# Kernel tuning notes

Hardware: AMD Instinct MI355X
Metric: run time of the kernel (lower is better)

Reference implementation:

```python
import jax, jax.numpy as jnp
import numpy as np

B, T, D = 2, 2048, 512
HEADS, DIM_HEAD, MAX_LAG = 8, 64, 5
INNER = HEADS * DIM_HEAD


def setup_inputs() -> dict:
    key = jax.random.key(0)
    k0, k1, k2, k3, k4 = jax.random.split(key, 5)
    x = jax.random.normal(k0, (B, T, D), dtype=jnp.float32)
    # Linear weights stored as (in, out); torch applies x @ W.T with W (out, in).
    Wq = jax.random.normal(k1, (D, INNER), dtype=jnp.float32) * (1.0 / np.sqrt(D))
    Wk = jax.random.normal(k2, (D, INNER), dtype=jnp.float32) * (1.0 / np.sqrt(D))
    Wv = jax.random.normal(k3, (D, INNER), dtype=jnp.float32) * (1.0 / np.sqrt(D))
    Wo = jax.random.normal(k4, (INNER, D), dtype=jnp.float32) * (1.0 / np.sqrt(INNER))
    bo = jnp.zeros((D,), dtype=jnp.float32)
    # Module's init: lag_weights = log(exp(-lags/(max_lag/3))) = -lags/(max_lag/3)
    lags = jnp.arange(MAX_LAG + 1, dtype=jnp.float32)
    lag_weights = jnp.broadcast_to(-(lags / (MAX_LAG / 3.0)), (HEADS, MAX_LAG + 1)).astype(jnp.float32)
    return {"x": x, "Wq": Wq, "Wk": Wk, "Wv": Wv, "Wo": Wo, "bo": bo, "lag_weights": lag_weights}


def reference(x, Wq, Wk, Wv, Wo, bo, lag_weights):
    b, t, _ = x.shape
    h, dh = HEADS, DIM_HEAD
    scale = dh ** -0.5
    # context defaults to x (self-attention)
    q = (x @ Wq).reshape(b, t, h, dh).transpose(0, 2, 1, 3)  # b h t d
    k = (x @ Wk).reshape(b, t, h, dh).transpose(0, 2, 1, 3)
    v = (x @ Wv).reshape(b, t, h, dh).transpose(0, 2, 1, 3)
    sim = jnp.einsum('bhid,bhjd->bhij', q, k) * scale  # b h t t
    # causal mask: keep j <= i
    causal = jnp.tril(jnp.ones((t, t), dtype=bool))
    neg = -jnp.finfo(sim.dtype).max
    sim = jnp.where(causal[None, None], sim, neg)
    # learned additive time-lag bias: lag_adj[h,i,j] = softmax(lag_weights)[h, clamp(i-j,0,MAX_LAG)]
    ti = jnp.arange(t)
    time_lags = jnp.clip(ti[:, None] - ti[None, :], 0, MAX_LAG)  # t t
    lag_probs = jax.nn.softmax(lag_weights, axis=-1)  # h (L+1)
    lag_adj = lag_probs[:, time_lags]  # h t t
    sim = sim + lag_adj[None]
    attn = jax.nn.softmax(sim, axis=-1)
    out = jnp.einsum('bhij,bhjd->bhid', attn, v)
    out = out.transpose(0, 2, 1, 3).reshape(b, t, h * dh)  # b t inner
    return out @ Wo + bo  # dropout is identity at eval
```

## Files before the change

### kernel.cpp

```cpp
#include <hip/hip_runtime.h>
#include <hip/hip_bf16.h>

#define BB 2
#define TT 2048
#define DD 512
#define HH 8
#define DH 64
#define INNER 512
#define MAXLAG 5

typedef __attribute__((ext_vector_type(8))) short short8;
typedef __attribute__((ext_vector_type(4))) float floatx4;
typedef unsigned short ushort_t;

__device__ inline unsigned short f2bf(float f) {
    unsigned u = __float_as_uint(f);
    unsigned r = (u + 0x7FFFu + ((u >> 16) & 1u)) >> 16;
    return (unsigned short)r;
}
__device__ inline float bf2f(unsigned short u) {
    return __uint_as_float(((unsigned)u) << 16);
}

__device__ __forceinline__ void gload16(ushort_t* lds, const ushort_t* g) {
    __builtin_amdgcn_global_load_lds(
        (const __attribute__((address_space(1))) void*)g,
        (__attribute__((address_space(3))) void*)lds, 16, 0, 0);
}

__global__ __launch_bounds__(256)
void cvt_kernel(const float* __restrict__ x,
                const float* __restrict__ wq, const float* __restrict__ wk,
                const float* __restrict__ wv, const float* __restrict__ wo,
                ushort_t* __restrict__ xb,
                ushort_t* __restrict__ wqkvt, ushort_t* __restrict__ wot)
{
    __shared__ float T[32][33];
    const int bid = blockIdx.x;
    if (bid < 1024) {
        int off = (bid * 256 + threadIdx.x) * 8;
        float4 a = *(const float4*)&x[off];
        float4 b = *(const float4*)&x[off + 4];
        ushort_t t[8];
        t[0] = f2bf(a.x); t[1] = f2bf(a.y); t[2] = f2bf(a.z); t[3] = f2bf(a.w);
        t[4] = f2bf(b.x); t[5] = f2bf(b.y); t[6] = f2bf(b.z); t[7] = f2bf(b.w);
        *(uint4*)&xb[off] = *(const uint4*)t;
        return;
    }
    const int r = bid - 1024;
    const int z = r >> 8;
    const int tile = r & 255;
    const float* s = (z == 0) ? wq : (z == 1) ? wk : (z == 2) ? wv : wo;
    ushort_t*    d = (z < 3) ? (wqkvt + (size_t)z * 512 * 512) : wot;
    const int k0 = (tile & 15) * 32;
    const int n0 = (tile >> 4) * 32;
    {
        const int kk = threadIdx.x >> 3;
        const int n4 = (threadIdx.x & 7) * 4;
        float4 v = *(const float4*)&s[(size_t)(k0 + kk) * 512 + n0 + n4];
        T[kk][n4 + 0] = v.x; T[kk][n4 + 1] = v.y;
        T[kk][n4 + 2] = v.z; T[kk][n4 + 3] = v.w;
    }
    __syncthreads();
    {
        const int nn = threadIdx.x >> 3;
        const int k4 = (threadIdx.x & 7) * 4;
        ushort4 o;
        o.x = f2bf(T[k4 + 0][nn]); o.y = f2bf(T[k4 + 1][nn]);
        o.z = f2bf(T[k4 + 2][nn]); o.w = f2bf(T[k4 + 3][nn]);
        *(ushort4*)&d[(size_t)(n0 + nn) * 512 + k0 + k4] = o;
    }
}

#define QM 128
#define QN 64
#define QKS 64

__global__ __launch_bounds__(256)
void gemm_qkv(const ushort_t* __restrict__ A, const ushort_t* __restrict__ Bw,
              ushort_t* __restrict__ q, ushort_t* __restrict__ k,
              ushort_t* __restrict__ vt)
{
    __shared__ ushort_t As[QM * QKS];
    __shared__ ushort_t Bs[QN * QKS];

    const int tid  = threadIdx.x;
    const int wave = tid >> 6;
    const int lane = tid & 63;
    const int quad = lane >> 4;
    const int l15  = lane & 15;
    const int wr   = wave >> 1;
    const int wc   = wave & 1;
    const int bm   = blockIdx.y * QM;
    const int bn   = blockIdx.x * QN;

    const int ga = wave * 256 + lane;
    const ushort_t* ap0 = &A[(size_t)(bm + ((ga +   0) >> 3)) * DD + ((ga +   0) & 7) * 8];
    const ushort_t* ap1 = &A[(size_t)(bm + ((ga +  64) >> 3)) * DD + ((ga +  64) & 7) * 8];
    const ushort_t* ap2 = &A[(size_t)(bm + ((ga + 128) >> 3)) * DD + ((ga + 128) & 7) * 8];
    const ushort_t* ap3 = &A[(size_t)(bm + ((ga + 192) >> 3)) * DD + ((ga + 192) & 7) * 8];
    const int gb = wave * 128 + lane;
    const ushort_t* bp0 = &Bw[(size_t)(bn + ((gb +  0) >> 3)) * DD + ((gb +  0) & 7) * 8];
    const ushort_t* bp1 = &Bw[(size_t)(bn + ((gb + 64) >> 3)) * DD + ((gb + 64) & 7) * 8];
    ushort_t* lA0 = &As[(size_t)(wave * 256 +   0) * 8];
    ushort_t* lA1 = &As[(size_t)(wave * 256 +  64) * 8];
    ushort_t* lA2 = &As[(size_t)(wave * 256 + 128) * 8];
    ushort_t* lA3 = &As[(size_t)(wave * 256 + 192) * 8];
    ushort_t* lB0 = &Bs[(size_t)(wave * 128 +  0) * 8];
    ushort_t* lB1 = &Bs[(size_t)(wave * 128 + 64) * 8];

    floatx4 acc[4][2];
#pragma unroll
    for (int i = 0; i < 4; ++i)
#pragma unroll
        for (int j = 0; j < 2; ++j) acc[i][j] = (floatx4){0.f, 0.f, 0.f, 0.f};

    for (int k0 = 0; k0 < DD; k0 += QKS) {
        __syncthreads();
        gload16(lA0, ap0 + k0);
        gload16(lA1, ap1 + k0);
        gload16(lA2, ap2 + k0);
        gload16(lA3, ap3 + k0);
        gload16(lB0, bp0 + k0);
        gload16(lB1, bp1 + k0);
        __syncthreads();

#pragma unroll
        for (int kk = 0; kk < 2; ++kk) {
            short8 af[4], bfr[2];
#pragma unroll
            for (int mt = 0; mt < 4; ++mt)
                af[mt] = *(const short8*)
                    &As[(((wr * 64 + mt * 16 + l15) << 3) + (kk << 2) + quad) * 8];
#pragma unroll
            for (int nt = 0; nt < 2; ++nt)
                bfr[nt] = *(const short8*)
                    &Bs[(((wc * 32 + nt * 16 + l15) << 3) + (kk << 2) + quad) * 8];
#pragma unroll
            for (int mt = 0; mt < 4; ++mt)
#pragma unroll
                for (int nt = 0; nt < 2; ++nt)
                    acc[mt][nt] = __builtin_amdgcn_mfma_f32_16x16x32_bf16(
                        af[mt], bfr[nt], acc[mt][nt], 0, 0, 0);
        }
    }

    const int z = bn >> 9;
    if (z == 2) {
#pragma unroll
        for (int mt = 0; mt < 4; ++mt) {
            const int m0 = bm + wr * 64 + mt * 16 + quad * 4;
            const int b  = m0 >> 11;
            const int t0 = m0 & 2047;
#pragma unroll
            for (int nt = 0; nt < 2; ++nt) {
                const int n  = bn + wc * 32 + nt * 16 + l15 - 1024;
                const int h  = n >> 6, dd = n & 63;
                ushort4 o;
                o.x = f2bf(acc[mt][nt][0]); o.y = f2bf(acc[mt][nt][1]);
                o.z = f2bf(acc[mt][nt][2]); o.w = f2bf(acc[mt][nt][3]);
                *(ushort4*)&vt[((size_t)((b * 8 + h) * 64 + dd)) * 2048 + t0] = o;
            }
        }
        return;
    }
    ushort_t* O = (z == 0) ? q : k;
    const int nb = bn - z * 512;
#pragma unroll
    for (int mt = 0; mt < 4; ++mt) {
#pragma unroll
        for (int nt = 0; nt < 2; ++nt) {
            const int n = nb + wc * 32 + nt * 16 + l15;
#pragma unroll
            for (int reg = 0; reg < 4; ++reg) {
                const int m = bm + wr * 64 + mt * 16 + quad * 4 + reg;
                O[(size_t)m * 512 + n] = f2bf(acc[mt][nt][reg]);
            }
        }
    }
}

__global__ __launch_bounds__(256)
void gemm_proj(const ushort_t* __restrict__ A, const ushort_t* __restrict__ Bw,
               float* __restrict__ O, const float* __restrict__ bias)
{
    __shared__ ushort_t As[64 * 64];
    __shared__ ushort_t Bs[64 * 64];

    const int tid  = threadIdx.x;
    const int wave = tid >> 6;
    const int lane = tid & 63;
    const int quad = lane >> 4;
    const int l15  = lane & 15;
    const int wr   = wave >> 1;
    const int wc   = wave & 1;
    const int bm   = blockIdx.y * 64;
    const int bn   = blockIdx.x * 64;

    const int g0 = wave * 128 + lane;
    const ushort_t* ap0 = &A[(size_t)(bm + ((g0 +  0) >> 3)) * INNER + ((g0 +  0) & 7) * 8];
    const ushort_t* ap1 = &A[(size_t)(bm + ((g0 + 64) >> 3)) * INNER + ((g0 + 64) & 7) * 8];
    const ushort_t* bp0 = &Bw[(size_t)(bn + ((g0 +  0) >> 3)) * INNER + ((g0 +  0) & 7) * 8];
    const ushort_t* bp1 = &Bw[(size_t)(bn + ((g0 + 64) >> 3)) * INNER + ((g0 + 64) & 7) * 8];
    ushort_t* lA0 = &As[(size_t)(wave * 128 +  0) * 8];
    ushort_t* lA1 = &As[(size_t)(wave * 128 + 64) * 8];
    ushort_t* lB0 = &Bs[(size_t)(wave * 128 +  0) * 8];
    ushort_t* lB1 = &Bs[(size_t)(wave * 128 + 64) * 8];

    floatx4 acc[2][2];
#pragma unroll
    for (int i = 0; i < 2; ++i)
#pragma unroll
        for (int j = 0; j < 2; ++j) acc[i][j] = (floatx4){0.f, 0.f, 0.f, 0.f};

    for (int k0 = 0; k0 < INNER; k0 += 64) {
        __syncthreads();
        gload16(lA0, ap0 + k0);
        gload16(lA1, ap1 + k0);
        gload16(lB0, bp0 + k0);
        gload16(lB1, bp1 + k0);
        __syncthreads();

#pragma unroll
        for (int kk = 0; kk < 2; ++kk) {
            short8 af[2], bfr[2];
#pragma unroll
            for (int mt = 0; mt < 2; ++mt)
                af[mt] = *(const short8*)
                    &As[(((wr * 32 + mt * 16 + l15) << 3) + (kk << 2) + quad) * 8];
#pragma unroll
            for (int nt = 0; nt < 2; ++nt)
                bfr[nt] = *(const short8*)
                    &Bs[(((wc * 32 + nt * 16 + l15) << 3) + (kk << 2) + quad) * 8];
#pragma unroll
            for (int mt = 0; mt < 2; ++mt)
#pragma unroll
                for (int nt = 0; nt < 2; ++nt)
                    acc[mt][nt] = __builtin_amdgcn_mfma_f32_16x16x32_bf16(
                        af[mt], bfr[nt], acc[mt][nt], 0, 0, 0);
        }
    }

    float bv[2];
#pragma unroll
    for (int nt = 0; nt < 2; ++nt)
        bv[nt] = bias[bn + wc * 32 + nt * 16 + l15];
#pragma unroll
    for (int mt = 0; mt < 2; ++mt) {
#pragma unroll
        for (int nt = 0; nt < 2; ++nt) {
            const int n = bn + wc * 32 + nt * 16 + l15;
#pragma unroll
            for (int reg = 0; reg < 4; ++reg) {
                const int m = bm + wr * 32 + mt * 16 + quad * 4 + reg;
                O[(size_t)m * 512 + n] = acc[mt][nt][reg] + bv[nt];
            }
        }
    }
}

#define PAD 72
#define MFIX 10.0f

__global__ __launch_bounds__(256)
void attn_mfma(const ushort_t* __restrict__ Qg,
               const ushort_t* __restrict__ Kg,
               const ushort_t* __restrict__ Vtg,
               const float* __restrict__ lagw,
               ushort_t* __restrict__ Opart,
               float* __restrict__ Lpart)
{
    __shared__ ushort_t Ks[64 * 8 * 8];
    __shared__ ushort_t Vts[64 * 8 * 8];
    __shared__ ushort_t Pl[4][16][PAD];

    const int tid  = threadIdx.x;
    const int wave = tid >> 6;
    const int lane = tid & 63;
    const int quad = lane >> 4;
    const int l15  = lane & 15;

    const int f  = blockIdx.x;
    const int rr = f >> 4;
    const int bh = f & 15;
    int qt, ci;
    if (rr < 32)      { qt = 31 - (rr >> 2); ci = rr & 3; }
    else if (rr < 56) { const int t = rr - 32; qt = 23 - t / 3; ci = t % 3; }
    else if (rr < 72) { const int t = rr - 56; qt = 15 - (t >> 1); ci = t & 1; }
    else              { qt = 79 - rr; ci = 0; }
    const int lo = ci * 8;
    const int hi = min(lo + 8, qt + 1);

    const int b  = bh >> 3;
    const int h  = bh & 7;
    const int i0 = qt * 64;

    float lagb[MAXLAG + 1];
    {
        float mx = -1e30f;
#pragma unroll
        for (int l = 0; l <= MAXLAG; ++l) {
            lagb[l] = lagw[h * (MAXLAG + 1) + l];
            mx = fmaxf(mx, lagb[l]);
        }
        float s = 0.f;
#pragma unroll
        for (int l = 0; l <= MAXLAG; ++l) { lagb[l] = __expf(lagb[l] - mx); s += lagb[l]; }
        float inv = 1.f / s;
#pragma unroll
        for (int l = 0; l <= MAXLAG; ++l) lagb[l] = lagb[l] * inv - MFIX;
    }
    const float c1  = 0.125f;
    const float c2f = lagb[MAXLAG];

    short8 qf0, qf1;
    {
        const ushort_t* qbase =
            Qg + ((size_t)(b * TT + i0 + wave * 16 + l15)) * INNER + h * DH;
        qf0 = *(const short8*)(qbase + quad * 8);
        qf1 = *(const short8*)(qbase + 32 + quad * 8);
    }

    floatx4 oacc[4];
    float lsum[4] = {0.f, 0.f, 0.f, 0.f};
#pragma unroll
    for (int cb = 0; cb < 4; ++cb) oacc[cb] = (floatx4){0.f, 0.f, 0.f, 0.f};

    const int ibase = i0 + wave * 16 + quad * 4;

    const int srow = tid >> 3;
    const int sc   = tid & 7;
    const ushort_t* Kp0 = Kg + ((size_t)(b * TT) + srow) * INNER + h * DH + sc * 8;
    const ushort_t* Kp1 = Kp0 + (size_t)32 * INNER;
    const ushort_t* Vp0 = Vtg + ((size_t)(bh * 64 + srow)) * 2048 + sc * 8;
    const ushort_t* Vp1 = Vp0 + (size_t)32 * 2048;
    const int slot = (sc + srow) & 7;
    const int kdst0 = ((srow << 3) + slot) << 3;
    const int kdst1 = (((srow + 32) << 3) + slot) << 3;

    uint4 pk0, pk1, pv0, pv1;
    {
        const size_t koff = (size_t)(lo * 64) * INNER;
        pk0 = *(const uint4*)(Kp0 + koff);
        pk1 = *(const uint4*)(Kp1 + koff);
        pv0 = *(const uint4*)(Vp0 + lo * 64);
        pv1 = *(const uint4*)(Vp1 + lo * 64);
    }

    for (int kt = lo; kt < hi; ++kt) {
        __syncthreads();
        *(uint4*)&Ks[kdst0]  = pk0;
        *(uint4*)&Ks[kdst1]  = pk1;
        *(uint4*)&Vts[kdst0] = pv0;
        *(uint4*)&Vts[kdst1] = pv1;
        if (kt + 1 < hi) {
            const size_t koff = (size_t)((kt + 1) * 64) * INNER;
            pk0 = *(const uint4*)(Kp0 + koff);
            pk1 = *(const uint4*)(Kp1 + koff);
            pv0 = *(const uint4*)(Vp0 + (kt + 1) * 64);
            pv1 = *(const uint4*)(Vp1 + (kt + 1) * 64);
        }
        __syncthreads();

        const int j0 = kt * 64;

        floatx4 sacc[4];
#pragma unroll
        for (int cb = 0; cb < 4; ++cb) {
            const int key = cb * 16 + l15;
            short8 kf0 = *(const short8*)&Ks[((key << 3) + ((quad + key) & 7)) << 3];
            short8 kf1 = *(const short8*)&Ks[((key << 3) + ((quad + 4 + key) & 7)) << 3];
            floatx4 zf = (floatx4){0.f, 0.f, 0.f, 0.f};
            zf = __builtin_amdgcn_mfma_f32_16x16x32_bf16(qf0, kf0, zf, 0, 0, 0);
            zf = __builtin_amdgcn_mfma_f32_16x16x32_bf16(qf1, kf1, zf, 0, 0, 0);
            sacc[cb] = zf;
        }

        float p[4][4];
        if (i0 + wave * 16 - (j0 + 63) >= MAXLAG) {
#pragma unroll
            for (int cb = 0; cb < 4; ++cb)
#pragma unroll
                for (int reg = 0; reg < 4; ++reg)
                    p[cb][reg] = __expf(fmaf(sacc[cb][reg], c1, c2f));
        } else {
#pragma unroll
            for (int cb = 0; cb < 4; ++cb) {
                const int j = j0 + cb * 16 + l15;
#pragma unroll
                for (int reg = 0; reg < 4; ++reg) {
                    const int lag = (ibase + reg) - j;
                    float bias = (lag <= 0) ? lagb[0]
                               : (lag == 1) ? lagb[1]
                               : (lag == 2) ? lagb[2]
                               : (lag == 3) ? lagb[3]
                               : (lag == 4) ? lagb[4] : lagb[5];
                    float e = __expf(fmaf(sacc[cb][reg], c1, bias));
                    p[cb][reg] = (lag < 0) ? 0.f : e;
                }
            }
        }
#pragma unroll
        for (int cb = 0; cb < 4; ++cb)
#pragma unroll
            for (int reg = 0; reg < 4; ++reg)
                lsum[reg] += p[cb][reg];

#pragma unroll
        for (int cb = 0; cb < 4; ++cb)
#pragma unroll
            for (int reg = 0; reg < 4; ++reg)
                Pl[wave][quad * 4 + reg][cb * 16 + l15] = f2bf(p[cb][reg]);

        short8 pf0 = *(const short8*)&Pl[wave][l15][quad * 8];
        short8 pf1 = *(const short8*)&Pl[wave][l15][32 + quad * 8];

#pragma unroll
        for (int cb = 0; cb < 4; ++cb) {
            const int dd = cb * 16 + l15;
            short8 vf0 = *(const short8*)&Vts[((dd << 3) + ((quad + dd) & 7)) << 3];
            short8 vf1 = *(const short8*)&Vts[((dd << 3) + ((quad + 4 + dd) & 7)) << 3];
            oacc[cb] = __builtin_amdgcn_mfma_f32_16x16x32_bf16(pf0, vf0, oacc[cb], 0, 0, 0);
            oacc[cb] = __builtin_amdgcn_mfma_f32_16x16x32_bf16(pf1, vf1, oacc[cb], 0, 0, 0);
        }
    }

#pragma unroll
    for (int reg = 0; reg < 4; ++reg) {
        lsum[reg] += __shfl_xor(lsum[reg], 1);
        lsum[reg] += __shfl_xor(lsum[reg], 2);
        lsum[reg] += __shfl_xor(lsum[reg], 4);
        lsum[reg] += __shfl_xor(lsum[reg], 8);
    }

#pragma unroll
    for (int reg = 0; reg < 4; ++reg) {
        const int row = ibase + reg;
        const size_t obase = ((size_t)(ci * 16 + bh) * TT + row) * 64;
#pragma unroll
        for (int cb = 0; cb < 4; ++cb)
            Opart[obase + cb * 16 + l15] = f2bf(oacc[cb][reg]);
        if (l15 == 0)
            Lpart[(size_t)(ci * 16 + bh) * TT + row] = lsum[reg];
    }
}

#define CMB_UNITS (16 * TT * 16)

__global__ __launch_bounds__(256)
void combine_kernel(const ushort_t* __restrict__ Opart,
                    const float* __restrict__ Lpart,
                    ushort_t* __restrict__ ao)
{
    int u = blockIdx.x * 256 + threadIdx.x;
    const int bh  = u >> 15;
    const int rem = u & 32767;
    const int i   = rem >> 4;
    const int d   = (rem & 15) * 4;
    const int b   = bh >> 3;
    const int h   = bh & 7;
    const int nch = ((i >> 6) >> 3) + 1;

    float s0 = 0.f, s1 = 0.f, s2 = 0.f, s3 = 0.f, l = 0.f;
    for (int ci = 0; ci < nch; ++ci) {
        const size_t p = ((size_t)(ci * 16 + bh) * TT + i) * 64 + d;
        ushort4 a = *(const ushort4*)&Opart[p];
        s0 += bf2f(a.x); s1 += bf2f(a.y); s2 += bf2f(a.z); s3 += bf2f(a.w);
        l  += Lpart[(size_t)(ci * 16 + bh) * TT + i];
    }
    const float inv = 1.f / l;
    ushort4 o;
    o.x = f2bf(s0 * inv);
    o.y = f2bf(s1 * inv);
    o.z = f2bf(s2 * inv);
    o.w = f2bf(s3 * inv);
    *(ushort4*)&ao[((size_t)(b * TT + i)) * INNER + h * DH + d] = o;
}

extern "C" void kernel_launch(void* const* d_in, const int* in_sizes, int n_in,
                              void* d_out, int out_size, void* d_ws, size_t ws_size,
                              hipStream_t stream)
{
    const float* x  = (const float*)d_in[0];
    const float* Wq = (const float*)d_in[1];
    const float* Wk = (const float*)d_in[2];
    const float* Wv = (const float*)d_in[3];
    const float* Wo = (const float*)d_in[4];
    const float* bo = (const float*)d_in[5];
    const float* lw = (const float*)d_in[6];
    float* out = (float*)d_out;

    const size_t SZ  = (size_t)BB * TT * INNER;
    const size_t NWE = (size_t)DD * INNER;
    ushort_t* xb    = (ushort_t*)d_ws;
    ushort_t* wqkvt = xb + SZ;
    ushort_t* wot   = wqkvt + 3 * NWE;
    ushort_t* q     = wot + NWE;
    ushort_t* k     = q + SZ;
    ushort_t* vt    = k + SZ;
    ushort_t* opart = vt + SZ;
    float*    lpart = (float*)(opart + 4 * (size_t)16 * TT * 64);
    ushort_t* ao    = xb;

    cvt_kernel<<<2048, 256, 0, stream>>>(x, Wq, Wk, Wv, Wo, xb, wqkvt, wot);

    dim3 gQKV(3 * INNER / QN, (BB * TT) / QM);
    gemm_qkv<<<gQKV, 256, 0, stream>>>(xb, wqkvt, q, k, vt);

    attn_mfma<<<1280, 256, 0, stream>>>(q, k, vt, lw, opart, lpart);

    combine_kernel<<<CMB_UNITS / 256, 256, 0, stream>>>(opart, lpart, ao);

    dim3 gPRJ(DD / 64, (BB * TT) / 64);
    gemm_proj<<<gPRJ, 256, 0, stream>>>(ao, wot, out, bo);
}
```

Measured before the change: 128.9 us.

## Fuse split-KV combine into attention via last-block atomic counter

Removes the separate combine kernel. Query tiles with a single KV chunk now normalize and write the output directly. For multi-chunk tiles, each block writes its partial result, increments a per-tile atomic counter, and the last block to arrive reduces all partials into the output. The counters are zeroed by an extra block in the conversion kernel. The GEMM K-loops are also fully unrolled. This saves one kernel launch and the full pass over partials for short rows, at the cost of threadfence/atomic overhead and a serialized tail reduction in the last block.

```diff
diff --git a/kernel.cpp b/kernel.cpp
--- a/kernel.cpp
+++ b/kernel.cpp
@@ -33,10 +33,16 @@
                 const float* __restrict__ wq, const float* __restrict__ wk,
                 const float* __restrict__ wv, const float* __restrict__ wo,
                 ushort_t* __restrict__ xb,
-                ushort_t* __restrict__ wqkvt, ushort_t* __restrict__ wot)
+                ushort_t* __restrict__ wqkvt, ushort_t* __restrict__ wot,
+                int* __restrict__ cnt)
 {
     __shared__ float T[32][33];
     const int bid = blockIdx.x;
+    if (bid >= 2048) {
+        if (threadIdx.x < 128)
+            ((int4*)cnt)[threadIdx.x] = (int4){0, 0, 0, 0};
+        return;
+    }
     if (bid < 1024) {
         int off = (bid * 256 + threadIdx.x) * 8;
         float4 a = *(const float4*)&x[off];
@@ -115,6 +121,7 @@
 #pragma unroll
         for (int j = 0; j < 2; ++j) acc[i][j] = (floatx4){0.f, 0.f, 0.f, 0.f};
 
+#pragma unroll
     for (int k0 = 0; k0 < DD; k0 += QKS) {
         __syncthreads();
         gload16(lA0, ap0 + k0);
@@ -213,6 +220,7 @@
 #pragma unroll
         for (int j = 0; j < 2; ++j) acc[i][j] = (floatx4){0.f, 0.f, 0.f, 0.f};
 
+#pragma unroll
     for (int k0 = 0; k0 < INNER; k0 += 64) {
         __syncthreads();
         gload16(lA0, ap0 + k0);
@@ -268,11 +276,14 @@
                const ushort_t* __restrict__ Vtg,
                const float* __restrict__ lagw,
                ushort_t* __restrict__ Opart,
-               float* __restrict__ Lpart)
+               float* __restrict__ Lpart,
+               int* __restrict__ cnt,
+               ushort_t* __restrict__ ao)
 {
     __shared__ ushort_t Ks[64 * 8 * 8];
     __shared__ ushort_t Vts[64 * 8 * 8];
     __shared__ ushort_t Pl[4][16][PAD];
+    __shared__ int lastFlag;
 
     const int tid  = threadIdx.x;
     const int wave = tid >> 6;
@@ -290,6 +301,7 @@
     else              { qt = 79 - rr; ci = 0; }
     const int lo = ci * 8;
     const int hi = min(lo + 8, qt + 1);
+    const int nch = (qt >> 3) + 1;
 
     const int b  = bh >> 3;
     const int h  = bh & 7;
@@ -433,6 +445,19 @@
         lsum[reg] += __shfl_xor(lsum[reg], 8);
     }
 
+    if (nch == 1) {
+#pragma unroll
+        for (int reg = 0; reg < 4; ++reg) {
+            const int row = ibase + reg;
+            const float inv = 1.f / lsum[reg];
+            ushort_t* dst = &ao[((size_t)(b * TT + row)) * INNER + h * DH];
+#pragma unroll
+            for (int cb = 0; cb < 4; ++cb)
+                dst[cb * 16 + l15] = f2bf(oacc[cb][reg] * inv);
+        }
+        return;
+    }
+
 #pragma unroll
     for (int reg = 0; reg < 4; ++reg) {
         const int row = ibase + reg;
@@ -443,38 +468,33 @@
         if (l15 == 0)
             Lpart[(size_t)(ci * 16 + bh) * TT + row] = lsum[reg];
     }
-}
-
-#define CMB_UNITS (16 * TT * 16)
-
-__global__ __launch_bounds__(256)
-void combine_kernel(const ushort_t* __restrict__ Opart,
-                    const float* __restrict__ Lpart,
-                    ushort_t* __restrict__ ao)
-{
-    int u = blockIdx.x * 256 + threadIdx.x;
-    const int bh  = u >> 15;
-    const int rem = u & 32767;
-    const int i   = rem >> 4;
-    const int d   = (rem & 15) * 4;
-    const int b   = bh >> 3;
-    const int h   = bh & 7;
-    const int nch = ((i >> 6) >> 3) + 1;
-
-    float s0 = 0.f, s1 = 0.f, s2 = 0.f, s3 = 0.f, l = 0.f;
-    for (int ci = 0; ci < nch; ++ci) {
-        const size_t p = ((size_t)(ci * 16 + bh) * TT + i) * 64 + d;
-        ushort4 a = *(const ushort4*)&Opart[p];
-        s0 += bf2f(a.x); s1 += bf2f(a.y); s2 += bf2f(a.z); s3 += bf2f(a.w);
-        l  += Lpart[(size_t)(ci * 16 + bh) * TT + i];
-    }
-    const float inv = 1.f / l;
-    ushort4 o;
-    o.x = f2bf(s0 * inv);
-    o.y = f2bf(s1 * inv);
-    o.z = f2bf(s2 * inv);
-    o.w = f2bf(s3 * inv);
-    *(ushort4*)&ao[((size_t)(b * TT + i)) * INNER + h * DH + d] = o;
+
+    __threadfence();
+    __syncthreads();
+    if (tid == 0)
+        lastFlag = (atomicAdd(&cnt[bh * 32 + qt], 1) == nch - 1);
+    __syncthreads();
+    if (!lastFlag) return;
+    __threadfence();
+
+    for (int u = tid; u < 1024; u += 256) {
+        const int i = i0 + (u >> 4);
+        const int d = (u & 15) * 4;
+        float s0 = 0.f, s1 = 0.f, s2 = 0.f, s3 = 0.f, l = 0.f;
+        for (int c2 = 0; c2 < nch; ++c2) {
+            const size_t p = ((size_t)(c2 * 16 + bh) * TT + i) * 64 + d;
+            ushort4 a = *(const ushort4*)&Opart[p];
+            s0 += bf2f(a.x); s1 += bf2f(a.y); s2 += bf2f(a.z); s3 += bf2f(a.w);
+            l  += Lpart[(size_t)(c2 * 16 + bh) * TT + i];
+        }
+        const float inv = 1.f / l;
+        ushort4 o;
+        o.x = f2bf(s0 * inv);
+        o.y = f2bf(s1 * inv);
+        o.z = f2bf(s2 * inv);
+        o.w = f2bf(s3 * inv);
+        *(ushort4*)&ao[((size_t)(b * TT + i)) * INNER + h * DH + d] = o;
+    }
 }
 
 extern "C" void kernel_launch(void* const* d_in, const int* in_sizes, int n_in,
@@ -500,16 +520,15 @@
     ushort_t* vt    = k + SZ;
     ushort_t* opart = vt + SZ;
     float*    lpart = (float*)(opart + 4 * (size_t)16 * TT * 64);
+    int*      cnt   = (int*)(lpart + 4 * (size_t)16 * TT);
     ushort_t* ao    = xb;
 
-    cvt_kernel<<<2048, 256, 0, stream>>>(x, Wq, Wk, Wv, Wo, xb, wqkvt, wot);
+    cvt_kernel<<<2049, 256, 0, stream>>>(x, Wq, Wk, Wv, Wo, xb, wqkvt, wot, cnt);
 
     dim3 gQKV(3 * INNER / QN, (BB * TT) / QM);
     gemm_qkv<<<gQKV, 256, 0, stream>>>(xb, wqkvt, q, k, vt);
 
-    attn_mfma<<<1280, 256, 0, stream>>>(q, k, vt, lw, opart, lpart);
-
-    combine_kernel<<<CMB_UNITS / 256, 256, 0, stream>>>(opart, lpart, ao);
+    attn_mfma<<<1280, 256, 0, stream>>>(q, k, vt, lw, opart, lpart, cnt, ao);
 
     dim3 gPRJ(DD / 64, (BB * TT) / 64);
     gemm_proj<<<gPRJ, 256, 0, stream>>>(ao, wot, out, bo);
```

Result: slower. 315.5 us (+144.8%).
